# Kernel optimization log

Measured on AMD Instinct MI355X. Metric: run time of the kernel, lower is better.

## Reference

```python
import jax, jax.numpy as jnp
import numpy as np

N = 300000        # occupied voxels
G = 128           # voxel grid side
C_IN = 128
C_OUT = 32
TIMES = C_IN // C_OUT
K = 27            # 3^3 kernel offsets


def _build_kernel_map():
    """Sample N unique voxels in a G^3 grid and build the 27-offset neighbor map.
    nbr[k, n] = index of the voxel at coords[n] + offset[k], or N if absent."""
    rng = np.random.default_rng(0)
    lin = rng.choice(G ** 3, size=N, replace=False).astype(np.int64)
    coords = np.stack(np.unravel_index(lin, (G, G, G)), axis=1).astype(np.int64)  # [N,3]
    lookup = np.full(G ** 3, N, dtype=np.int32)
    lookup[lin] = np.arange(N, dtype=np.int32)
    offs = np.stack(np.meshgrid(*[[-1, 0, 1]] * 3, indexing='ij'), axis=-1).reshape(-1, 3)  # [27,3]
    nbr = np.empty((K, N), dtype=np.int32)
    for k, off in enumerate(offs):
        nc = coords + off
        valid = np.all((nc >= 0) & (nc < G), axis=1)
        li = (nc[:, 0] * G + nc[:, 1]) * G + nc[:, 2]
        nbr[k] = np.where(valid, lookup[np.clip(li, 0, G ** 3 - 1)], N)
    return nbr


def setup_inputs() -> dict:
    key = jax.random.key(0)
    k1, k2, k3, k4 = jax.random.split(key, 4)
    feats = jax.random.normal(k1, (N, C_IN), dtype=jnp.float32)
    W0 = jax.random.normal(k2, (K, C_IN, C_IN), dtype=jnp.float32) * 0.05
    W1 = jax.random.normal(k3, (K, C_IN, C_OUT), dtype=jnp.float32) * 0.05
    W2 = jax.random.normal(k4, (K, C_OUT, C_OUT), dtype=jnp.float32) * 0.05
    nbr_idx = jnp.asarray(_build_kernel_map())
    return {"feats": feats, "W0": W0, "W1": W1, "W2": W2, "nbr_idx": nbr_idx}


def sparse_conv(x, W, nbr):
    """Gather-GEMM-accumulate sparse conv: out[n] = sum_k x[nbr[k,n]] @ W[k].
    Missing neighbors (index N) gather a zero row."""
    xp = jnp.concatenate([x, jnp.zeros((1, x.shape[1]), x.dtype)], axis=0)  # [N+1,Cin]
    out0 = jnp.zeros((x.shape[0], W.shape[2]), x.dtype)

    def body(acc, kw):
        idx, Wk = kw
        return acc + xp[idx] @ Wk, None

    out, _ = jax.lax.scan(body, out0, (nbr, W))
    return out


def reference(feats, W0, W1, W2, nbr_idx):
    n = feats.shape[0]
    # mean over channel groups: [N, times, C_out] -> [N, C_out]
    downsampled = jnp.mean(feats.reshape(n, TIMES, C_OUT), axis=1)
    upsampled = jnp.tile(downsampled, (1, TIMES))           # [N, C_in]
    residual = feats - upsampled
    residual = sparse_conv(residual, W0, nbr_idx)           # C_in -> C_in
    residual = sparse_conv(residual, W1, nbr_idx)           # C_in -> C_out
    residual = sparse_conv(residual, W2, nbr_idx)           # C_out -> C_out
    return downsampled + residual
```

## Files before the change

kernel.cpp:

```cpp
#include <hip/hip_runtime.h>

#define DEVINL __device__ __forceinline__

typedef __attribute__((ext_vector_type(8))) __bf16 bf16x8;
typedef __attribute__((ext_vector_type(4))) float f32x4;
typedef __attribute__((ext_vector_type(8))) unsigned short u16x8;

DEVINL unsigned short f2bf(float x) {
  unsigned u = __builtin_bit_cast(unsigned, x);
  u += 0x7FFFu + ((u >> 16) & 1u);
  return (unsigned short)(u >> 16);
}

#define BARRIER() asm volatile("s_barrier" ::: "memory")

template <int N>
DEVINL void waitvm() {
  asm volatile("s_waitcnt vmcnt(%0)" ::"n"(N) : "memory");
}

DEVINL void gload16(const void* g, void* l) {
  __builtin_amdgcn_global_load_lds(
      (const __attribute__((address_space(1))) void*)g,
      (__attribute__((address_space(3))) void*)l, 16, 0, 0);
}

__global__ __launch_bounds__(256) void prep_kernel(
    const float* __restrict__ F, unsigned short* __restrict__ RES,
    float* __restrict__ DS, int n) {
  const int t = threadIdx.x;
  const int row = blockIdx.x * 16 + (t >> 4);
  const int cg = t & 15;
  if (row >= n) return;
  const float4* f4 = (const float4*)(F + (size_t)row * 128 + cg * 8);
  float4 v0 = f4[0], v1 = f4[1];
  float v[8] = {v0.x, v0.y, v0.z, v0.w, v1.x, v1.y, v1.z, v1.w};
  float s[8] = {v0.x, v0.y, v0.z, v0.w, v1.x, v1.y, v1.z, v1.w};
#pragma unroll
  for (int i = 0; i < 8; ++i) s[i] += __shfl_xor(s[i], 4);
#pragma unroll
  for (int i = 0; i < 8; ++i) s[i] += __shfl_xor(s[i], 8);
  u16x8 rb;
#pragma unroll
  for (int i = 0; i < 8; ++i) rb[i] = f2bf(v[i] - 0.25f * s[i]);
  *(u16x8*)(RES + (size_t)row * 128 + cg * 8) = rb;
  if (cg < 4) {
    float4 d0 = {0.25f * s[0], 0.25f * s[1], 0.25f * s[2], 0.25f * s[3]};
    float4 d1 = {0.25f * s[4], 0.25f * s[5], 0.25f * s[6], 0.25f * s[7]};
    float4* dp = (float4*)(DS + (size_t)row * 32 + cg * 8);
    dp[0] = d0;
    dp[1] = d1;
  }
}

template <int CIN, int COUT>
DEVINL void pack_one(const float* __restrict__ W, unsigned short* __restrict__ P, int g) {
  const int n = g % COUT;
  const int t = g / COUT;
  const int q = t & 3;
  const int t2 = t >> 2;
  const int ks = t2 % (CIN / 32);
  const int k = t2 / (CIN / 32);
  const float* src = W + ((size_t)k * CIN + ks * 32 + q * 8) * COUT + n;
  unsigned short* dst = P + (size_t)g * 8;
#pragma unroll
  for (int j = 0; j < 8; ++j) dst[j] = f2bf(src[(size_t)j * COUT]);
}

__global__ __launch_bounds__(256) void pack_kernel(
    const float* __restrict__ W0, const float* __restrict__ W1,
    const float* __restrict__ W2, unsigned short* __restrict__ P0,
    unsigned short* __restrict__ P1, unsigned short* __restrict__ P2) {
  int g = blockIdx.x * 256 + threadIdx.x;
  if (g < 55296)
    pack_one<128, 128>(W0, P0, g);
  else if (g < 69120)
    pack_one<128, 32>(W1, P1, g - 55296);
  else if (g < 72576)
    pack_one<32, 32>(W2, P2, g - 69120);
}

__global__ void zero_tail(unsigned short* a, unsigned short* b, unsigned short* c) {
  int t = threadIdx.x;
  if (t < 128) { a[t] = 0; b[t] = 0; }
  if (t < 32) c[t] = 0;
}

template <int CIN, int COUT, int BK, int BM, int WM, int WN, bool FINAL, int MINB>
__global__ __launch_bounds__(256, MINB) void spconv(
    const unsigned short* __restrict__ X, const unsigned short* __restrict__ Bp,
    const int* __restrict__ nbr, unsigned short* __restrict__ Y,
    float* __restrict__ OUT, const float* __restrict__ DS, int nr) {
  constexpr int H = CIN / BK;
  constexpr int S = 27 * H;
  constexpr int NBUF = 3;
  constexpr int KSL = BK / 32;
  constexpr int WROWS = BM / WM;
  constexpr int WCOLS = COUT / WN;
  constexpr int MF = WROWS / 16;
  constexpr int NF = WCOLS / 16;
  constexpr int CPR = BK / 8;
  constexpr int SWZ = (CPR < 8 ? CPR - 1 : 7);
  constexpr int RB = BK * 2;
  constexpr int APF = BM * CPR / 256;
  constexpr int NB = KSL * NF;

  __shared__ unsigned short As[NBUF][BM * BK];
  __shared__ int IdxS[28 * BM];

  const int tid = threadIdx.x;
  const int lane = tid & 63;
  const int wave = tid >> 6;
  const int wm = wave / WN;
  const int wn = wave % WN;
  const int base = blockIdx.x * BM;
  const int q = lane >> 4;
  const int l16 = lane & 15;

  for (int f = tid; f < 28 * BM; f += 256) {
    int k = f / BM;
    int nn = base + (f % BM);
    IdxS[f] = (k < 27 && nn < nr) ? nbr[(size_t)k * nr + nn] : nr;
  }
  __syncthreads();

  const unsigned short* bbase = Bp + ((size_t)q * COUT + wn * WCOLS + l16) * 8;

  bf16x8 bA[NB], bB[NB];

  auto loadB = [&](bf16x8(&dst)[NB], int s) {
    const int k0 = s / H;
    const int k = (k0 > 26) ? 26 : k0;
    const int hh = s % H;
#pragma unroll
    for (int ks = 0; ks < KSL; ++ks)
#pragma unroll
      for (int j = 0; j < NF; ++j) {
        const int ksg = hh * KSL + ks;
        dst[ks * NF + j] = *(const bf16x8*)(
            bbase + ((size_t)k * CIN * COUT) + ((size_t)(ksg * 4) * COUT + j * 16) * 8);
      }
  };

  auto issueA = [&](int s) {
    const int k = s / H;
    const int hh = s % H;
    const int kb = s % NBUF;
#pragma unroll
    for (int pp = 0; pp < APF; ++pp) {
      int slot = pp * 256 + tid;
      int r = slot / CPR;
      int cc = (slot % CPR) * 16;
      int csw = cc ^ ((r & SWZ) << 4);
      int g = IdxS[k * BM + r];
      gload16(X + (size_t)g * CIN + hh * BK + (csw >> 1),
              (char*)(&As[kb][0]) + slot * 16);
    }
  };

  f32x4 acc[MF][NF] = {};

  auto mfmaStep = [&](int kb, const bf16x8(&bf)[NB]) {
    const char* Ab = (const char*)(&As[kb][0]);
#pragma unroll
    for (int ks = 0; ks < KSL; ++ks) {
      bf16x8 af[MF];
#pragma unroll
      for (int i = 0; i < MF; ++i) {
        int r = wm * WROWS + i * 16 + l16;
        int db = r * RB + (((ks * 64 + q * 16) & (RB - 1)) ^ ((r & SWZ) << 4));
        af[i] = __builtin_bit_cast(bf16x8, *(const uint4*)(Ab + db));
      }
#pragma unroll
      for (int i = 0; i < MF; ++i)
#pragma unroll
        for (int j = 0; j < NF; ++j)
          acc[i][j] = __builtin_amdgcn_mfma_f32_16x16x32_bf16(af[i], bf[ks * NF + j],
                                                              acc[i][j], 0, 0, 0);
    }
  };

  issueA(0);
  loadB(bA, 0);

#pragma unroll 1
  for (int s = 0; s + 1 < S; s += 2) {
    loadB(bB, s + 1);
    issueA(s + 1);
    waitvm<NB + APF>();
    BARRIER();
    mfmaStep(s % NBUF, bA);
    loadB(bA, s + 2);
    issueA(s + 2);
    waitvm<NB + APF>();
    BARRIER();
    mfmaStep((s + 1) % NBUF, bB);
  }
  waitvm<0>();
  if constexpr (S & 1) {
    BARRIER();
    mfmaStep((S - 1) % NBUF, bA);
  }

#pragma unroll
  for (int i = 0; i < MF; ++i)
#pragma unroll
    for (int j = 0; j < NF; ++j)
#pragma unroll
      for (int r = 0; r < 4; ++r) {
        int row = base + wm * WROWS + i * 16 + q * 4 + r;
        int col = wn * WCOLS + j * 16 + l16;
        if (row < nr) {
          float v = acc[i][j][r];
          if constexpr (FINAL)
            OUT[(size_t)row * COUT + col] = v + DS[(size_t)row * COUT + col];
          else
            Y[(size_t)row * COUT + col] = f2bf(v);
        }
      }
}

template <int CIN, int COUT, int BK, int BM, int WM, int WN, bool FINAL, int MINB>
__global__ __launch_bounds__(256, MINB) void spconv_reg(
    const unsigned short* __restrict__ X, const unsigned short* __restrict__ Bp,
    const int* __restrict__ nbr, unsigned short* __restrict__ Y,
    float* __restrict__ OUT, const float* __restrict__ DS, int nr) {
  constexpr int H = CIN / BK;
  constexpr int S = 27 * H;
  constexpr int KSL = BK / 32;
  constexpr int WROWS = BM / WM;
  constexpr int WCOLS = COUT / WN;
  constexpr int MF = WROWS / 16;
  constexpr int NF = WCOLS / 16;
  constexpr int NB = KSL * NF;
  constexpr int AL = MF * KSL;

  __shared__ int IdxS[28 * BM];

  const int tid = threadIdx.x;
  const int lane = tid & 63;
  const int wave = tid >> 6;
  const int wm = wave / WN;
  const int wn = wave % WN;
  const int base = blockIdx.x * BM;
  const int q = lane >> 4;
  const int l16 = lane & 15;

  for (int f = tid; f < 28 * BM; f += 256) {
    int k = f / BM;
    int nn = base + (f % BM);
    IdxS[f] = (k < 27 && nn < nr) ? nbr[(size_t)k * nr + nn] : nr;
  }
  __syncthreads();

  const unsigned short* bbase = Bp + ((size_t)q * COUT + wn * WCOLS + l16) * 8;

  bf16x8 bA[NB], bB[NB], aA[AL], aB[AL];

  auto loadB = [&](bf16x8(&dst)[NB], int s) {
    const int k0 = s / H;
    const int k = (k0 > 26) ? 26 : k0;
    const int hh = s % H;
#pragma unroll
    for (int ks = 0; ks < KSL; ++ks)
#pragma unroll
      for (int j = 0; j < NF; ++j) {
        const int ksg = hh * KSL + ks;
        dst[ks * NF + j] = *(const bf16x8*)(
            bbase + ((size_t)k * CIN * COUT) + ((size_t)(ksg * 4) * COUT + j * 16) * 8);
      }
  };

  auto loadA = [&](bf16x8(&dst)[AL], int s) {
    const int k = s / H;
    const int hh = s % H;
#pragma unroll
    for (int i = 0; i < MF; ++i) {
      int r = wm * WROWS + i * 16 + l16;
      int g = IdxS[k * BM + r];
      const unsigned short* src = X + (size_t)g * CIN + hh * BK + q * 8;
#pragma unroll
      for (int ks = 0; ks < KSL; ++ks)
        dst[i * KSL + ks] = *(const bf16x8*)(src + ks * 32);
    }
  };

  f32x4 acc[MF][NF] = {};

  auto mfmaStep = [&](const bf16x8(&af)[AL], const bf16x8(&bf)[NB]) {
#pragma unroll
    for (int ks = 0; ks < KSL; ++ks)
#pragma unroll
      for (int i = 0; i < MF; ++i)
#pragma unroll
        for (int j = 0; j < NF; ++j)
          acc[i][j] = __builtin_amdgcn_mfma_f32_16x16x32_bf16(
              af[i * KSL + ks], bf[ks * NF + j], acc[i][j], 0, 0, 0);
  };

  loadB(bA, 0);
  loadA(aA, 0);

#pragma unroll 1
  for (int s = 0; s + 1 < S; s += 2) {
    loadB(bB, s + 1);
    loadA(aB, s + 1);
    waitvm<NB + AL>();
    mfmaStep(aA, bA);
    loadB(bA, s + 2);
    loadA(aA, s + 2);
    waitvm<NB + AL>();
    mfmaStep(aB, bB);
  }
  if constexpr (S & 1) {
    waitvm<0>();
    mfmaStep(aA, bA);
  }

#pragma unroll
  for (int i = 0; i < MF; ++i)
#pragma unroll
    for (int j = 0; j < NF; ++j)
#pragma unroll
      for (int r = 0; r < 4; ++r) {
        int row = base + wm * WROWS + i * 16 + q * 4 + r;
        int col = wn * WCOLS + j * 16 + l16;
        if (row < nr) {
          float v = acc[i][j][r];
          if constexpr (FINAL)
            OUT[(size_t)row * COUT + col] = v + DS[(size_t)row * COUT + col];
          else
            Y[(size_t)row * COUT + col] = f2bf(v);
        }
      }
}

extern "C" void kernel_launch(void* const* d_in, const int* in_sizes, int n_in,
                              void* d_out, int out_size, void* d_ws, size_t ws_size,
                              hipStream_t stream) {
  const float* feats = (const float*)d_in[0];
  const float* W0 = (const float*)d_in[1];
  const float* W1 = (const float*)d_in[2];
  const float* W2 = (const float*)d_in[3];
  const int* nbr = (const int*)d_in[4];
  const int n = in_sizes[0] / 128;
  float* out = (float*)d_out;

  char* p = (char*)d_ws;
  auto take = [&](size_t bytes) {
    char* r = p;
    p += (bytes + 255) & ~(size_t)255;
    return r;
  };
  unsigned short* resB = (unsigned short*)take((size_t)(n + 1) * 128 * 2);
  unsigned short* y0 = (unsigned short*)take((size_t)(n + 1) * 128 * 2);
  unsigned short* y1 = (unsigned short*)take((size_t)(n + 1) * 32 * 2);
  float* ds = (float*)take((size_t)n * 32 * 4);
  unsigned short* p0 = (unsigned short*)take((size_t)27 * 128 * 128 * 2);
  unsigned short* p1 = (unsigned short*)take((size_t)27 * 128 * 32 * 2);
  unsigned short* p2 = (unsigned short*)take((size_t)27 * 32 * 32 * 2);

  prep_kernel<<<(n + 15) / 16, 256, 0, stream>>>(feats, resB, ds, n);
  pack_kernel<<<284, 256, 0, stream>>>(W0, W1, W2, p0, p1, p2);
  zero_tail<<<1, 128, 0, stream>>>(resB + (size_t)n * 128, y0 + (size_t)n * 128,
                                   y1 + (size_t)n * 32);
  const int gb128 = (n + 127) / 128;
  spconv<128, 128, 64, 128, 1, 4, false, 2>
      <<<gb128, 256, 0, stream>>>(resB, p0, nbr, y0, nullptr, nullptr, n);
  spconv_reg<128, 32, 64, 128, 4, 1, false, 3>
      <<<gb128, 256, 0, stream>>>(y0, p1, nbr, y1, nullptr, nullptr, n);
  spconv_reg<32, 32, 32, 128, 4, 1, true, 4>
      <<<gb128, 256, 0, stream>>>(y1, p2, nbr, nullptr, out, ds, n);
}
```

Before: 570.5 us.

## Prefetch neighbor indices into registers instead of LDS table in first conv

The first sparse conv kernel drops the per-block LDS table of 28×BM neighbor indices and its up-front fill plus syncthreads. Indices are now loaded from global memory into registers two stages ahead and pipelined alongside the A and B loads, with the vmcnt wait adjusted for the extra loads. This frees about 14 KB of LDS, which is why the launch bound rises from 2 to 3 blocks per CU to gain occupancy. The cost is more registers and extra global index loads in the hot loop, and the odd-S tail step is removed on the assumption that S is even.

```diff
diff --git a/kernel.cpp b/kernel.cpp
--- a/kernel.cpp
+++ b/kernel.cpp
@@ -86,8 +86,8 @@
   if (t < 32) c[t] = 0;
 }
 
-template <int CIN, int COUT, int BK, int BM, int WM, int WN, bool FINAL, int MINB>
-__global__ __launch_bounds__(256, MINB) void spconv(
+template <int CIN, int COUT, int BK, int BM, int WN, bool FINAL, int MINB>
+__global__ __launch_bounds__(256, MINB) void spconv0(
     const unsigned short* __restrict__ X, const unsigned short* __restrict__ Bp,
     const int* __restrict__ nbr, unsigned short* __restrict__ Y,
     float* __restrict__ OUT, const float* __restrict__ DS, int nr) {
@@ -95,38 +95,30 @@
   constexpr int S = 27 * H;
   constexpr int NBUF = 3;
   constexpr int KSL = BK / 32;
-  constexpr int WROWS = BM / WM;
   constexpr int WCOLS = COUT / WN;
-  constexpr int MF = WROWS / 16;
+  constexpr int MF = BM / 16;
   constexpr int NF = WCOLS / 16;
   constexpr int CPR = BK / 8;
-  constexpr int SWZ = (CPR < 8 ? CPR - 1 : 7);
+  constexpr int SWZ = 7;
   constexpr int RB = BK * 2;
   constexpr int APF = BM * CPR / 256;
   constexpr int NB = KSL * NF;
+  constexpr int WAITN = NB + 2 * APF;
 
   __shared__ unsigned short As[NBUF][BM * BK];
-  __shared__ int IdxS[28 * BM];
 
   const int tid = threadIdx.x;
   const int lane = tid & 63;
   const int wave = tid >> 6;
-  const int wm = wave / WN;
-  const int wn = wave % WN;
+  const int wn = wave;
   const int base = blockIdx.x * BM;
   const int q = lane >> 4;
   const int l16 = lane & 15;
 
-  for (int f = tid; f < 28 * BM; f += 256) {
-    int k = f / BM;
-    int nn = base + (f % BM);
-    IdxS[f] = (k < 27 && nn < nr) ? nbr[(size_t)k * nr + nn] : nr;
-  }
-  __syncthreads();
-
   const unsigned short* bbase = Bp + ((size_t)q * COUT + wn * WCOLS + l16) * 8;
 
   bf16x8 bA[NB], bB[NB];
+  int iv0[APF], iv1[APF];
 
   auto loadB = [&](bf16x8(&dst)[NB], int s) {
     const int k0 = s / H;
@@ -142,8 +134,21 @@
       }
   };
 
-  auto issueA = [&](int s) {
+  auto loadIdx = [&](int(&iv)[APF], int s) {
     const int k = s / H;
+    const bool kok = k < 27;
+    const int kc = kok ? k : 0;
+#pragma unroll
+    for (int pp = 0; pp < APF; ++pp) {
+      int r = pp * 32 + (tid >> 3);
+      int nn = base + r;
+      bool ok = kok && (nn < nr);
+      int a = nbr[(size_t)kc * nr + (ok ? nn : 0)];
+      iv[pp] = ok ? a : nr;
+    }
+  };
+
+  auto issueA = [&](int s, const int(&iv)[APF]) {
     const int hh = s % H;
     const int kb = s % NBUF;
 #pragma unroll
@@ -152,8 +157,7 @@
       int r = slot / CPR;
       int cc = (slot % CPR) * 16;
       int csw = cc ^ ((r & SWZ) << 4);
-      int g = IdxS[k * BM + r];
-      gload16(X + (size_t)g * CIN + hh * BK + (csw >> 1),
+      gload16(X + (size_t)iv[pp] * CIN + hh * BK + (csw >> 1),
               (char*)(&As[kb][0]) + slot * 16);
     }
   };
@@ -167,7 +171,7 @@
       bf16x8 af[MF];
 #pragma unroll
       for (int i = 0; i < MF; ++i) {
-        int r = wm * WROWS + i * 16 + l16;
+        int r = i * 16 + l16;
         int db = r * RB + (((ks * 64 + q * 16) & (RB - 1)) ^ ((r & SWZ) << 4));
         af[i] = __builtin_bit_cast(bf16x8, *(const uint4*)(Ab + db));
       }
@@ -180,27 +184,28 @@
     }
   };
 
-  issueA(0);
+  loadIdx(iv0, 0);
+  loadIdx(iv1, 1);
+  issueA(0, iv0);
+  loadIdx(iv0, 2);
   loadB(bA, 0);
 
 #pragma unroll 1
   for (int s = 0; s + 1 < S; s += 2) {
     loadB(bB, s + 1);
-    issueA(s + 1);
-    waitvm<NB + APF>();
+    issueA(s + 1, iv1);
+    loadIdx(iv1, s + 3);
+    waitvm<WAITN>();
     BARRIER();
     mfmaStep(s % NBUF, bA);
     loadB(bA, s + 2);
-    issueA(s + 2);
-    waitvm<NB + APF>();
+    issueA(s + 2, iv0);
+    loadIdx(iv0, s + 4);
+    waitvm<WAITN>();
     BARRIER();
     mfmaStep((s + 1) % NBUF, bB);
   }
   waitvm<0>();
-  if constexpr (S & 1) {
-    BARRIER();
-    mfmaStep((S - 1) % NBUF, bA);
-  }
 
 #pragma unroll
   for (int i = 0; i < MF; ++i)
@@ -208,7 +213,7 @@
     for (int j = 0; j < NF; ++j)
 #pragma unroll
       for (int r = 0; r < 4; ++r) {
-        int row = base + wm * WROWS + i * 16 + q * 4 + r;
+        int row = base + i * 16 + q * 4 + r;
         int col = wn * WCOLS + j * 16 + l16;
         if (row < nr) {
           float v = acc[i][j][r];
@@ -365,7 +370,7 @@
   zero_tail<<<1, 128, 0, stream>>>(resB + (size_t)n * 128, y0 + (size_t)n * 128,
                                    y1 + (size_t)n * 32);
   const int gb128 = (n + 127) / 128;
-  spconv<128, 128, 64, 128, 1, 4, false, 2>
+  spconv0<128, 128, 64, 128, 4, false, 3>
       <<<gb128, 256, 0, stream>>>(resB, p0, nbr, y0, nullptr, nullptr, n);
   spconv_reg<128, 32, 64, 128, 4, 1, false, 3>
       <<<gb128, 256, 0, stream>>>(y0, p1, nbr, y1, nullptr, nullptr, n);
```

Measured after the change: 548.4 us. 1.04x faster.
